# Kernel optimization log

Hardware: AMD Instinct MI355X
Metric: run time of the kernel (lower is better)

## Reference

```python
import jax, jax.numpy as jnp
import numpy as np

N = 8192
IN_F = 512
OUT_F = 64
NEG_INF = -9e15

def setup_inputs() -> dict:
    key = jax.random.key(0)
    k1, k2, k3, k4 = jax.random.split(key, 4)
    node_features = jax.random.normal(k1, (N, IN_F), dtype=jnp.float32)
    adjacency_matrix = jax.random.randint(k2, (N, N), 0, 2, dtype=jnp.int32)
    # Xavier-uniform-like init (gain 1.414), scale irrelevant for correctness
    w_bound = 1.414 * np.sqrt(6.0 / (IN_F + OUT_F))
    a_bound = 1.414 * np.sqrt(6.0 / (2 * OUT_F + 1))
    weight_matrix = jax.random.uniform(k3, (IN_F, OUT_F), minval=-w_bound, maxval=w_bound, dtype=jnp.float32)
    attention_vector = jax.random.uniform(k4, (2 * OUT_F, 1), minval=-a_bound, maxval=a_bound, dtype=jnp.float32)
    return {
        "node_features": node_features,
        "adjacency_matrix": adjacency_matrix,
        "weight_matrix": weight_matrix,
        "attention_vector": attention_vector,
    }

def reference(node_features, adjacency_matrix, weight_matrix, attention_vector):
    # h: [N, F] transformed features
    h = node_features @ weight_matrix
    # score[i, j] = h[i] . a_left + h[j] . a_right
    a_left = attention_vector[:OUT_F, 0]   # [F]
    a_right = attention_vector[OUT_F:, 0]  # [F]
    scores = (h @ a_left)[:, None] + (h @ a_right)[None, :]  # [N, N]
    # NOTE: source defines leaky_relu but never applies it in forward — faithful omission.
    masked = jnp.where(adjacency_matrix > 0, scores, NEG_INF)
    attn = jax.nn.softmax(masked, axis=1)  # [N, N]
    # dropout p=0 / inference: no-op
    out = attn @ h  # [N, F]
    return jax.nn.elu(out)  # concat=True path
```

## Files before the change

### kernel.cpp

```cpp
#include <hip/hip_runtime.h>
#include <hip/hip_bf16.h>
#include <cstdint>

#define NN      8192
#define OF      64
#define KC      16
#define CW      512
#define ASTR    72
#define PSTR    65

#define OFF_HW  0
#define OFF_P   1310720

typedef __attribute__((ext_vector_type(8))) short  s16x8;
typedef __attribute__((ext_vector_type(4))) float  f32x4;

__device__ __forceinline__ unsigned short f2bf(float f) {
  unsigned int u = __float_as_uint(f);
  unsigned int r = (u + 0x7FFFu + ((u >> 16) & 1u)) >> 16;
  return (unsigned short)r;
}

__device__ __forceinline__ void lds_barrier() {
  __builtin_amdgcn_s_waitcnt(0xC07F);
  __builtin_amdgcn_s_barrier();
}

__global__ __launch_bounds__(256) void k1_hw(const float* __restrict__ X,
                                             const float* __restrict__ W,
                                             const float* __restrict__ att,
                                             unsigned short* __restrict__ HW) {
  __shared__ float xs[16 * 516];
  __shared__ float ws[64 * 68];
  int t = threadIdx.x;
  int rb = blockIdx.x * 16;

  {
    const float4* src = (const float4*)(X + (size_t)rb * 512);
#pragma unroll
    for (int s = 0; s < 8; ++s) {
      int lid = s * 256 + t;
      int row = lid >> 7, kseg = lid & 127;
      *(float4*)&xs[row * 516 + kseg * 4] = src[row * 128 + kseg];
    }
  }

  int row = t >> 4, tx = t & 15;
  float4 acc = {0.f, 0.f, 0.f, 0.f};
  for (int kc = 0; kc < 8; ++kc) {
    __syncthreads();
#pragma unroll
    for (int s = 0; s < 4; ++s) {
      int lid = s * 256 + t;
      int k = lid >> 4, cs = lid & 15;
      *(float4*)&ws[k * 68 + cs * 4] =
          *(const float4*)(W + (size_t)(kc * 64 + k) * 64 + cs * 4);
    }
    __syncthreads();
#pragma unroll 16
    for (int k = 0; k < 64; ++k) {
      float x = xs[row * 516 + kc * 64 + k];
      float4 w4 = *(const float4*)&ws[k * 68 + tx * 4];
      acc.x += x * w4.x; acc.y += x * w4.y;
      acc.z += x * w4.z; acc.w += x * w4.w;
    }
  }

  float v = acc.x * att[64 + tx * 4]     + acc.y * att[64 + tx * 4 + 1] +
            acc.z * att[64 + tx * 4 + 2] + acc.w * att[64 + tx * 4 + 3];
#pragma unroll
  for (int m = 8; m > 0; m >>= 1) v += __shfl_xor(v, m, 64);
  float e = expf(v);

  int j = rb + row;
  unsigned short* hw = HW + j;
  float hv[4] = {acc.x, acc.y, acc.z, acc.w};
#pragma unroll
  for (int c = 0; c < 4; ++c)
    hw[(size_t)(tx * 4 + c) * NN] = f2bf(e * hv[c]);
  if (tx == 0) hw[(size_t)64 * NN] = f2bf(e);
}

__global__ __launch_bounds__(256, 2) void k3_gat(const int* __restrict__ A,
                                                 const unsigned short* __restrict__ HW,
                                                 float* __restrict__ P) {
  __shared__ unsigned short bt[65 * 512];
  __shared__ unsigned short at[64 * ASTR];

  int t = threadIdx.x;
  int kc = blockIdx.x & 15;
  int mg = blockIdx.x >> 4;
  int lane = t & 63, w = t >> 6;
  int l15 = lane & 15, q = lane >> 4;
  int k0 = kc * CW;
  int rowM = mg * 64;

  const int* ap[4];
#pragma unroll
  for (int i = 0; i < 4; ++i)
    ap[i] = A + (size_t)(rowM + w * 16 + i * 4 + q) * NN + k0 + l15 * 4;

  int4 av[3][4];
#pragma unroll
  for (int i = 0; i < 4; ++i) av[0][i] = *(const int4*)(ap[i]);
#pragma unroll
  for (int i = 0; i < 4; ++i) av[1][i] = *(const int4*)(ap[i] + 64);

#pragma unroll
  for (int rds = 0; rds < 16; ++rds) {
    int lid = rds * 256 + t;
    int row = lid >> 6, ch = lid & 63;
    uint4 v = *(const uint4*)(HW + (size_t)row * NN + k0 + ch * 8);
    *(uint4*)&bt[row * 512 + ((ch ^ (row & 7)) * 8)] = v;
  }
  if (t < 64) {
    uint4 v = *(const uint4*)(HW + (size_t)64 * NN + k0 + t * 8);
    *(uint4*)&bt[64 * 512 + t * 8] = v;
  }

  int swz = l15 & 7;
  int bb[4][2];
#pragma unroll
  for (int tt = 0; tt < 4; ++tt)
#pragma unroll
    for (int ks = 0; ks < 2; ++ks)
      bb[tt][ks] = ((tt * 16 + l15) * 512 + (((ks * 4 + q) ^ swz) * 8)) * 2;
  int eb0 = (64 * 512 + q * 8) * 2;
  int eb1 = (64 * 512 + (4 + q) * 8) * 2;
  int ab  = ((w * 16 + l15) * ASTR + q * 8) * 2;

  f32x4 acc[5];
#pragma unroll
  for (int tt = 0; tt < 5; ++tt) acc[tt] = 0.f;
  const s16x8 zero8 = {0, 0, 0, 0, 0, 0, 0, 0};

#pragma unroll
  for (int s = 0; s < 8; ++s) {
    lds_barrier();
#pragma unroll
    for (int i = 0; i < 4; ++i) {
      int4 vv = av[s % 3][i];
      uint2 p;
      p.x = (unsigned)(vv.x | (vv.y << 16)) * 0x3F80u;
      p.y = (unsigned)(vv.z | (vv.w << 16)) * 0x3F80u;
      *(uint2*)((char*)at + (((w * 16 + i * 4 + q) * ASTR + l15 * 4) * 2)) = p;
    }
    if (s < 6) {
#pragma unroll
      for (int i = 0; i < 4; ++i)
        av[(s + 2) % 3][i] = *(const int4*)(ap[i] + (s + 2) * 64);
    }
    lds_barrier();

    s16x8 af0 = *(const s16x8*)((char*)at + ab);
    s16x8 af1 = *(const s16x8*)((char*)at + ab + 64);
    int so = s * 128;
#pragma unroll
    for (int ks = 0; ks < 2; ++ks) {
      s16x8 af = ks ? af1 : af0;
#pragma unroll
      for (int tt = 0; tt < 4; ++tt) {
        s16x8 b = *(const s16x8*)((char*)bt + bb[tt][ks] + so);
        acc[tt] = __builtin_amdgcn_mfma_f32_16x16x32_bf16(af, b, acc[tt], 0, 0, 0);
      }
      s16x8 b4 = *(const s16x8*)((char*)bt + (ks ? eb1 : eb0) + so);
      b4 = (l15 == 0) ? b4 : zero8;
      acc[4] = __builtin_amdgcn_mfma_f32_16x16x32_bf16(af, b4, acc[4], 0, 0, 0);
    }
  }

  float* Pp = P + (size_t)kc * NN * PSTR;
  int rb = rowM + w * 16 + q * 4;
#pragma unroll
  for (int tt = 0; tt < 4; ++tt)
#pragma unroll
    for (int rg = 0; rg < 4; ++rg)
      Pp[(size_t)(rb + rg) * PSTR + tt * 16 + l15] = acc[tt][rg];
  if (l15 == 0)
#pragma unroll
    for (int rg = 0; rg < 4; ++rg)
      Pp[(size_t)(rb + rg) * PSTR + 64] = acc[4][rg];
}

__global__ __launch_bounds__(256) void k4_fin(const float* __restrict__ P,
                                              float* __restrict__ out) {
  int g = blockIdx.x * 256 + threadIdx.x;
  int i = g >> 6, c = g & 63;
  float num = 0.f, S = 0.f;
#pragma unroll
  for (int kc = 0; kc < KC; ++kc) {
    const float* p = P + (size_t)kc * NN * PSTR + (size_t)i * PSTR;
    num += p[c];
    S   += p[64];
  }
  float x = num / S;
  out[g] = x > 0.f ? x : expm1f(x);
}

extern "C" void kernel_launch(void* const* d_in, const int* in_sizes, int n_in,
                              void* d_out, int out_size, void* d_ws, size_t ws_size,
                              hipStream_t stream) {
  const float* X  = (const float*)d_in[0];
  const int*   A  = (const int*)d_in[1];
  const float* W  = (const float*)d_in[2];
  const float* av = (const float*)d_in[3];
  float* out = (float*)d_out;

  char* ws = (char*)d_ws;
  unsigned short* HW = (unsigned short*)(ws + OFF_HW);
  float*          P  = (float*)(ws + OFF_P);

  k1_hw<<<NN / 16, 256, 0, stream>>>(X, W, av, HW);
  k3_gat<<<128 * KC, 256, 0, stream>>>(A, HW, P);
  k4_fin<<<(size_t)NN * OF / 256, 256, 0, stream>>>(P, out);
}
```

Before: 396.3 us.

## Pack adjacency into bitmask prepass and expand bits directly into MFMA A fragments

Adds a ballot-based kernel that compresses the int32 adjacency matrix into a 1-bit-per-entry mask. The main GAT kernel then reads mask bytes and expands them in registers into bf16 A fragments, which removes the LDS staging of the adjacency tile and its barriers. Each block now covers 128 rows instead of 64, so the shared HW tile is reused across two M-tiles and half as many blocks are launched. The full adjacency matrix still has to be read once by the pack kernel, and the extra launch and larger accumulator state add cost.

```diff
diff --git a/kernel.cpp b/kernel.cpp
--- a/kernel.cpp
+++ b/kernel.cpp
@@ -6,11 +6,12 @@
 #define OF      64
 #define KC      16
 #define CW      512
-#define ASTR    72
 #define PSTR    65
+#define RBYTES  1024
 
 #define OFF_HW  0
 #define OFF_P   1310720
+#define OFF_BM  35389440
 
 typedef __attribute__((ext_vector_type(8))) short  s16x8;
 typedef __attribute__((ext_vector_type(4))) float  f32x4;
@@ -21,9 +22,29 @@
   return (unsigned short)r;
 }
 
-__device__ __forceinline__ void lds_barrier() {
-  __builtin_amdgcn_s_waitcnt(0xC07F);
-  __builtin_amdgcn_s_barrier();
+__global__ __launch_bounds__(256) void ka_pack(const int* __restrict__ A,
+                                               unsigned long long* __restrict__ BM) {
+  int t = threadIdx.x;
+  int l = t & 63, w = t >> 6;
+  int row = blockIdx.x * 4 + w;
+  const int* ap = A + (size_t)row * NN;
+  unsigned long long* bp = BM + (size_t)row * (RBYTES / 8);
+#pragma unroll 4
+  for (int i = 0; i < 32; ++i) {
+    int base = i * 256;
+    int a0 = ap[base + l];
+    int a1 = ap[base + 64 + l];
+    int a2 = ap[base + 128 + l];
+    int a3 = ap[base + 192 + l];
+    unsigned long long w0 = __ballot(a0 > 0);
+    unsigned long long w1 = __ballot(a1 > 0);
+    unsigned long long w2 = __ballot(a2 > 0);
+    unsigned long long w3 = __ballot(a3 > 0);
+    if (l == 0) {
+      bp[i * 4 + 0] = w0; bp[i * 4 + 1] = w1;
+      bp[i * 4 + 2] = w2; bp[i * 4 + 3] = w3;
+    }
+  }
 }
 
 __global__ __launch_bounds__(256) void k1_hw(const float* __restrict__ X,
@@ -81,11 +102,18 @@
   if (tx == 0) hw[(size_t)64 * NN] = f2bf(e);
 }
 
-__global__ __launch_bounds__(256, 2) void k3_gat(const int* __restrict__ A,
+__device__ __forceinline__ s16x8 expand8(unsigned m) {
+  union { unsigned u[4]; s16x8 v; } r;
+#pragma unroll
+  for (int j = 0; j < 4; ++j)
+    r.u[j] = (((m >> (2 * j)) & 1u) | (((m >> (2 * j + 1)) & 1u) << 16)) * 0x3F80u;
+  return r.v;
+}
+
+__global__ __launch_bounds__(256, 2) void k3_gat(const unsigned char* __restrict__ BM,
                                                  const unsigned short* __restrict__ HW,
                                                  float* __restrict__ P) {
   __shared__ unsigned short bt[65 * 512];
-  __shared__ unsigned short at[64 * ASTR];
 
   int t = threadIdx.x;
   int kc = blockIdx.x & 15;
@@ -93,18 +121,7 @@
   int lane = t & 63, w = t >> 6;
   int l15 = lane & 15, q = lane >> 4;
   int k0 = kc * CW;
-  int rowM = mg * 64;
-
-  const int* ap[4];
-#pragma unroll
-  for (int i = 0; i < 4; ++i)
-    ap[i] = A + (size_t)(rowM + w * 16 + i * 4 + q) * NN + k0 + l15 * 4;
-
-  int4 av[3][4];
-#pragma unroll
-  for (int i = 0; i < 4; ++i) av[0][i] = *(const int4*)(ap[i]);
-#pragma unroll
-  for (int i = 0; i < 4; ++i) av[1][i] = *(const int4*)(ap[i] + 64);
+  int rowM = mg * 128;
 
 #pragma unroll
   for (int rds = 0; rds < 16; ++rds) {
@@ -117,6 +134,7 @@
     uint4 v = *(const uint4*)(HW + (size_t)64 * NN + k0 + t * 8);
     *(uint4*)&bt[64 * 512 + t * 8] = v;
   }
+  __syncthreads();
 
   int swz = l15 & 7;
   int bb[4][2];
@@ -127,59 +145,76 @@
       bb[tt][ks] = ((tt * 16 + l15) * 512 + (((ks * 4 + q) ^ swz) * 8)) * 2;
   int eb0 = (64 * 512 + q * 8) * 2;
   int eb1 = (64 * 512 + (4 + q) * 8) * 2;
-  int ab  = ((w * 16 + l15) * ASTR + q * 8) * 2;
-
-  f32x4 acc[5];
-#pragma unroll
-  for (int tt = 0; tt < 5; ++tt) acc[tt] = 0.f;
+
+  const unsigned char* bmr[2];
+#pragma unroll
+  for (int mt = 0; mt < 2; ++mt)
+    bmr[mt] = BM + (size_t)(rowM + w * 32 + mt * 16 + l15) * RBYTES + kc * 64 + q;
+
+  f32x4 acc[2][5];
+#pragma unroll
+  for (int mt = 0; mt < 2; ++mt)
+#pragma unroll
+    for (int tt = 0; tt < 5; ++tt) acc[mt][tt] = 0.f;
   const s16x8 zero8 = {0, 0, 0, 0, 0, 0, 0, 0};
 
+  unsigned c0[2], c1[2];
+#pragma unroll
+  for (int mt = 0; mt < 2; ++mt) { c0[mt] = bmr[mt][0]; c1[mt] = bmr[mt][4]; }
+
 #pragma unroll
   for (int s = 0; s < 8; ++s) {
-    lds_barrier();
-#pragma unroll
-    for (int i = 0; i < 4; ++i) {
-      int4 vv = av[s % 3][i];
-      uint2 p;
-      p.x = (unsigned)(vv.x | (vv.y << 16)) * 0x3F80u;
-      p.y = (unsigned)(vv.z | (vv.w << 16)) * 0x3F80u;
-      *(uint2*)((char*)at + (((w * 16 + i * 4 + q) * ASTR + l15 * 4) * 2)) = p;
-    }
-    if (s < 6) {
-#pragma unroll
-      for (int i = 0; i < 4; ++i)
-        av[(s + 2) % 3][i] = *(const int4*)(ap[i] + (s + 2) * 64);
-    }
-    lds_barrier();
-
-    s16x8 af0 = *(const s16x8*)((char*)at + ab);
-    s16x8 af1 = *(const s16x8*)((char*)at + ab + 64);
+    unsigned n0[2], n1[2];
+    if (s < 7) {
+#pragma unroll
+      for (int mt = 0; mt < 2; ++mt) {
+        n0[mt] = bmr[mt][(s + 1) * 8];
+        n1[mt] = bmr[mt][(s + 1) * 8 + 4];
+      }
+    }
+
+    s16x8 af[2][2];
+#pragma unroll
+    for (int mt = 0; mt < 2; ++mt) {
+      af[mt][0] = expand8(c0[mt]);
+      af[mt][1] = expand8(c1[mt]);
+    }
+
     int so = s * 128;
 #pragma unroll
     for (int ks = 0; ks < 2; ++ks) {
-      s16x8 af = ks ? af1 : af0;
 #pragma unroll
       for (int tt = 0; tt < 4; ++tt) {
         s16x8 b = *(const s16x8*)((char*)bt + bb[tt][ks] + so);
-        acc[tt] = __builtin_amdgcn_mfma_f32_16x16x32_bf16(af, b, acc[tt], 0, 0, 0);
+#pragma unroll
+        for (int mt = 0; mt < 2; ++mt)
+          acc[mt][tt] = __builtin_amdgcn_mfma_f32_16x16x32_bf16(af[mt][ks], b, acc[mt][tt], 0, 0, 0);
       }
       s16x8 b4 = *(const s16x8*)((char*)bt + (ks ? eb1 : eb0) + so);
       b4 = (l15 == 0) ? b4 : zero8;
-      acc[4] = __builtin_amdgcn_mfma_f32_16x16x32_bf16(af, b4, acc[4], 0, 0, 0);
-    }
+#pragma unroll
+      for (int mt = 0; mt < 2; ++mt)
+        acc[mt][4] = __builtin_amdgcn_mfma_f32_16x16x32_bf16(af[mt][ks], b4, acc[mt][4], 0, 0, 0);
+    }
+
+#pragma unroll
+    for (int mt = 0; mt < 2; ++mt) { c0[mt] = n0[mt]; c1[mt] = n1[mt]; }
   }
 
   float* Pp = P + (size_t)kc * NN * PSTR;
-  int rb = rowM + w * 16 + q * 4;
-#pragma unroll
-  for (int tt = 0; tt < 4; ++tt)
-#pragma unroll
-    for (int rg = 0; rg < 4; ++rg)
-      Pp[(size_t)(rb + rg) * PSTR + tt * 16 + l15] = acc[tt][rg];
-  if (l15 == 0)
-#pragma unroll
-    for (int rg = 0; rg < 4; ++rg)
-      Pp[(size_t)(rb + rg) * PSTR + 64] = acc[4][rg];
+#pragma unroll
+  for (int mt = 0; mt < 2; ++mt) {
+    int rb = rowM + w * 32 + mt * 16 + q * 4;
+#pragma unroll
+    for (int tt = 0; tt < 4; ++tt)
+#pragma unroll
+      for (int rg = 0; rg < 4; ++rg)
+        Pp[(size_t)(rb + rg) * PSTR + tt * 16 + l15] = acc[mt][tt][rg];
+    if (l15 == 0)
+#pragma unroll
+      for (int rg = 0; rg < 4; ++rg)
+        Pp[(size_t)(rb + rg) * PSTR + 64] = acc[mt][4][rg];
+  }
 }
 
 __global__ __launch_bounds__(256) void k4_fin(const float* __restrict__ P,
@@ -207,10 +242,12 @@
   float* out = (float*)d_out;
 
   char* ws = (char*)d_ws;
-  unsigned short* HW = (unsigned short*)(ws + OFF_HW);
-  float*          P  = (float*)(ws + OFF_P);
-
+  unsigned short*     HW = (unsigned short*)(ws + OFF_HW);
+  float*              P  = (float*)(ws + OFF_P);
+  unsigned long long* BM = (unsigned long long*)(ws + OFF_BM);
+
+  ka_pack<<<NN / 4, 256, 0, stream>>>(A, BM);
   k1_hw<<<NN / 16, 256, 0, stream>>>(X, W, av, HW);
-  k3_gat<<<128 * KC, 256, 0, stream>>>(A, HW, P);
+  k3_gat<<<64 * KC, 256, 0, stream>>>((const unsigned char*)BM, HW, P);
   k4_fin<<<(size_t)NN * OF / 256, 256, 0, stream>>>(P, out);
 }
```

Result: slower. 419.8 us (+5.9%).
